# Kernel optimization log

Hardware: AMD Instinct MI355X
Metric: run time of the kernel (lower is better)

Reference implementation:

```python
import jax, jax.numpy as jnp
import numpy as np

N_NODES = 100000
N_EDGES = 1600000
N_GRAPHS = 256
K_HOPS = 3


def setup_inputs() -> dict:
    key = jax.random.key(0)
    ks = jax.random.split(key, 10)
    x = jax.random.normal(ks[0], (N_NODES, 32), dtype=jnp.float32)
    edge_index = jax.random.randint(ks[1], (2, N_EDGES), 0, N_NODES, dtype=jnp.int32)
    batch = jnp.sort(jax.random.randint(ks[2], (N_NODES,), 0, N_GRAPHS, dtype=jnp.int32))
    gcn_w = jax.random.normal(ks[3], (64, 32), dtype=jnp.float32) * 0.1
    gcn_b = jax.random.normal(ks[4], (64,), dtype=jnp.float32) * 0.1
    w1 = jax.random.normal(ks[5], (32, 64), dtype=jnp.float32) * 0.1
    b1 = jax.random.normal(ks[6], (32,), dtype=jnp.float32) * 0.1
    w2 = jax.random.normal(ks[7], (16, 32), dtype=jnp.float32) * 0.1
    b2 = jax.random.normal(ks[8], (16,), dtype=jnp.float32) * 0.1
    return {"x": x, "edge_index": edge_index, "batch": batch,
            "gcn_w": gcn_w, "gcn_b": gcn_b, "w1": w1, "b1": b1, "w2": w2, "b2": b2}


def reference(x, edge_index, batch, gcn_w, gcn_b, w1, b1, w2, b2):
    N = x.shape[0]
    src, dst = edge_index[0], edge_index[1]
    # GCN symmetric normalization with self-loops: deg = in-degree + 1
    deg = jax.ops.segment_sum(jnp.ones_like(src, dtype=x.dtype), dst, num_segments=N) + 1.0
    norm = deg ** -0.5  # [N]
    h = x
    for _ in range(K_HOPS):
        # edge message: norm[src] * h[src], scattered to dst, scaled by norm[dst];
        # self-loop contributes norm[i]^2 * h[i]
        msg = h[src] * norm[src][:, None]                     # [E, C]
        agg = jax.ops.segment_sum(msg, dst, num_segments=N)    # [N, C]
        h = norm[:, None] * agg + (norm * norm)[:, None] * h
    h = jax.nn.relu(h @ gcn_w.T + gcn_b)                       # [N, hidden]
    # global mean pool per graph
    counts = jax.ops.segment_sum(jnp.ones((N,), x.dtype), batch, num_segments=N_GRAPHS)
    sums = jax.ops.segment_sum(h, batch, num_segments=N_GRAPHS)
    h_avg = sums / jnp.maximum(counts, 1.0)[:, None]           # [G, hidden]
    # classifier (dropout = identity in eval)
    h1 = jax.nn.relu(h_avg @ w1.T + b1)
    logits = h1 @ w2.T + b2                                    # [G, nc]
    return logits
```

## Files before the change

### kernel.cpp

```cpp
#include <hip/hip_runtime.h>

constexpr int NW    = 391;
constexpr int CH    = 8192;
constexpr int CAP_B = 8192;
constexpr int CAP_C = 10240;

__device__ __forceinline__ unsigned bf16_rne(float x) {
    unsigned u = __float_as_uint(x);
    u += 0x7fffu + ((u >> 16) & 1u);
    return u >> 16;
}
__device__ __forceinline__ unsigned pack2(float even, float odd) {
    return bf16_rne(even) | (bf16_rne(odd) << 16);
}
__device__ __forceinline__ float lo_f(unsigned u) { return __uint_as_float(u << 16); }
__device__ __forceinline__ float hi_f(unsigned u) { return __uint_as_float(u & 0xffff0000u); }


__global__ __launch_bounds__(512) void k_bucket(const int* __restrict__ src,
                                                const int* __restrict__ dst, int E,
                                                int* __restrict__ wcur, int* __restrict__ packed) {
    __shared__ int h[256];
    __shared__ int base[256];
    int t = threadIdx.x;
    if (t < 256) h[t] = 0;
    __syncthreads();
    int b0 = blockIdx.x * CH;
    int cnt = min(CH, E - b0);
    for (int i = t; i < cnt; i += 512) atomicAdd(&h[dst[b0 + i] / NW], 1);
    __syncthreads();
    if (t < 256) { base[t] = atomicAdd(&wcur[t], h[t]); h[t] = 0; }
    __syncthreads();
    for (int i = t; i < cnt; i += 512) {
        int d = dst[b0 + i];
        int s = src[b0 + i];
        int w = d / NW;
        int l = d - w * NW;
        int r = atomicAdd(&h[w], 1);
        int pos = base[w] + r;
        if (pos < CAP_B) packed[w * CAP_B + pos] = (l << 17) | s;
    }
}


__global__ __launch_bounds__(512) void k_window(const int* __restrict__ packed,
                                                const int* __restrict__ wcur,
                                                float* __restrict__ norm,
                                                int2* __restrict__ rng,
                                                int* __restrict__ csr, int N, int W) {
    __shared__ int hist[NW];
    __shared__ int scan[512];
    __shared__ int cur[NW];
    int t = threadIdx.x, w = blockIdx.x;
    int lo = w * NW, nwn = min(NW, N - lo);
    for (int i = t; i < NW; i += 512) hist[i] = 0;
    __syncthreads();
    int cnt = min(wcur[w], CAP_B);
    const int* pk = packed + (size_t)w * CAP_B;
    for (int e = t; e < cnt; e += 512) atomicAdd(&hist[pk[e] >> 17], 1);
    __syncthreads();
    int d = (t < nwn) ? hist[t] : 0;
    if (t < nwn) norm[lo + t] = rsqrtf((float)(d + 1));
    int pd = (t < nwn) ? ((d + 7) & ~7) : 0;
    scan[t] = pd;
    __syncthreads();
    for (int s = 1; s < 512; s <<= 1) {
        int add = (t >= s) ? scan[t - s] : 0;
        __syncthreads();
        scan[t] += add;
        __syncthreads();
    }
    int base = w * CAP_C;
    int cend = base + scan[t];
    if (t < nwn) {
        rng[lo + t] = make_int2(cend - pd, cend);
        cur[t] = cend - pd;
    }
    if (w == W - 1 && t == 0) { norm[N] = 1.f; rng[N] = make_int2(0, 0); }
    __syncthreads();
    for (int e = t; e < cnt; e += 512) {
        int p = pk[e];
        int pos = atomicAdd(&cur[p >> 17], 1);
        csr[pos] = p & 0x1FFFF;
    }
    __syncthreads();
    if (t < nwn) {
        for (int pos = cur[t]; pos < cend; ++pos) csr[pos] = N;
    }
}


__global__ void k_prep(const float4* __restrict__ x, const float* __restrict__ norm,
                       uint2* __restrict__ outb, int N) {
    int t = blockIdx.x * blockDim.x + threadIdx.x;
    int i = t >> 3;
    if (i < N) {
        float n = norm[i];
        float4 v = x[t];
        outb[t] = make_uint2(pack2(v.x * n, v.y * n), pack2(v.z * n, v.w * n));
    } else if (i == N) {
        outb[t] = make_uint2(0u, 0u);
    }
}

template <bool LAST>
__global__ void k_hop(const uint2* __restrict__ tab, const float* __restrict__ norm,
                      const int2* __restrict__ rng, const int* __restrict__ csr,
                      uint2* __restrict__ outb, float4* __restrict__ outf, int N) {
    int group = (blockIdx.x * blockDim.x + threadIdx.x) >> 3;
    int l = threadIdx.x & 7;
    if (group > N) return;
    uint2 sv = tab[(size_t)group * 8 + l];
    float ax = lo_f(sv.x), ay = hi_f(sv.x), az = lo_f(sv.y), aw = hi_f(sv.y);
    int2 be = rng[group];
    for (int k = be.x; k < be.y; k += 8) {
        int e = csr[k + l];
        uint2 u[8];
#pragma unroll
        for (int j = 0; j < 8; ++j) {
            int s = __shfl(e, j, 8);
            u[j] = tab[(size_t)s * 8 + l];
        }
#pragma unroll
        for (int j = 0; j < 8; ++j) {
            ax += lo_f(u[j].x); ay += hi_f(u[j].x);
            az += lo_f(u[j].y); aw += hi_f(u[j].y);
        }
    }
    float n = norm[group];
    float sc = LAST ? n : n * n;
    ax *= sc; ay *= sc; az *= sc; aw *= sc;
    if (LAST) {
        if (group < N) outf[(size_t)group * 8 + l] = make_float4(ax, ay, az, aw);
    } else {
        outb[(size_t)group * 8 + l] = make_uint2(pack2(ax, ay), pack2(az, aw));
    }
}


__global__ __launch_bounds__(256) void k_feat(const float4* __restrict__ h4,
                                              const float* __restrict__ gw,
                                              const float* __restrict__ gb,
                                              float4* __restrict__ z4, int N) {
    __shared__ float w[64 * 32];
    __shared__ float bs[64];
    int t = threadIdx.x;
    for (int i = t; i < 64 * 32; i += 256) w[i] = gw[i];
    if (t < 64) bs[t] = gb[t];
    __syncthreads();
    int n = blockIdx.x * 256 + t;
    if (n >= N) return;
    float hrow[32];
    const float4* hr = h4 + (size_t)n * 8;
#pragma unroll
    for (int q = 0; q < 8; ++q) {
        float4 v = hr[q];
        hrow[q * 4] = v.x; hrow[q * 4 + 1] = v.y; hrow[q * 4 + 2] = v.z; hrow[q * 4 + 3] = v.w;
    }
#pragma unroll
    for (int c0 = 0; c0 < 64; c0 += 16) {
        float o[16];
#pragma unroll
        for (int cc = 0; cc < 16; ++cc) {
            const float* wr = &w[(c0 + cc) * 32];
            float d = bs[c0 + cc];
#pragma unroll
            for (int k = 0; k < 32; ++k) d += hrow[k] * wr[k];
            o[cc] = fmaxf(d, 0.f);
        }
#pragma unroll
        for (int q = 0; q < 4; ++q)
            z4[(size_t)n * 16 + (c0 >> 2) + q] =
                make_float4(o[q * 4], o[q * 4 + 1], o[q * 4 + 2], o[q * 4 + 3]);
    }
}


__global__ __launch_bounds__(256) void k_pool(const float4* __restrict__ z4,
                                              const int* __restrict__ batch, int N,
                                              const float* __restrict__ w1, const float* __restrict__ b1,
                                              const float* __restrict__ w2, const float* __restrict__ b2,
                                              float* __restrict__ out) {
    __shared__ float4 part[16][17];
    __shared__ float havg[64];
    __shared__ float h1s[32];
    __shared__ int se[2];
    int t = threadIdx.x, g = blockIdx.x;
    if (t < 2) {
        int target = g + t;
        int lo = 0, hi = N;
        while (lo < hi) { int mid = (lo + hi) >> 1; if (batch[mid] < target) lo = mid + 1; else hi = mid; }
        se[t] = lo;
    }
    __syncthreads();
    int start = se[0], end = se[1];
    int q = t & 15;
    int r = t >> 4;
    float4 acc = make_float4(0.f, 0.f, 0.f, 0.f);
    for (int n = start + r; n < end; n += 16) {
        float4 v = z4[(size_t)n * 16 + q];
        acc.x += v.x; acc.y += v.y; acc.z += v.z; acc.w += v.w;
    }
    part[r][q] = acc;
    __syncthreads();
#pragma unroll
    for (int s = 8; s > 0; s >>= 1) {
        if (r < s) {
            float4 a = part[r][q], b = part[r + s][q];
            a.x += b.x; a.y += b.y; a.z += b.z; a.w += b.w;
            part[r][q] = a;
        }
        __syncthreads();
    }
    if (t < 16) {
        int cnt = end - start;
        float inv = 1.f / (float)(cnt > 0 ? cnt : 1);
        float4 a = part[0][t];
        havg[t * 4] = a.x * inv; havg[t * 4 + 1] = a.y * inv;
        havg[t * 4 + 2] = a.z * inv; havg[t * 4 + 3] = a.w * inv;
    }
    __syncthreads();
    if (t < 32) {
        float d = b1[t];
#pragma unroll
        for (int k = 0; k < 64; ++k) d += havg[k] * w1[t * 64 + k];
        h1s[t] = fmaxf(d, 0.f);
    }
    __syncthreads();
    if (t < 16) {
        float d = b2[t];
#pragma unroll
        for (int j = 0; j < 32; ++j) d += h1s[j] * w2[t * 32 + j];
        out[g * 16 + t] = d;
    }
}


extern "C" void kernel_launch(void* const* d_in, const int* in_sizes, int n_in,
                              void* d_out, int out_size, void* d_ws, size_t ws_size,
                              hipStream_t stream) {
    const float* x     = (const float*)d_in[0];
    const int*   ei    = (const int*)d_in[1];
    const int*   batch = (const int*)d_in[2];
    const float* gw    = (const float*)d_in[3];
    const float* gb    = (const float*)d_in[4];
    const float* w1    = (const float*)d_in[5];
    const float* b1    = (const float*)d_in[6];
    const float* w2    = (const float*)d_in[7];
    const float* b2    = (const float*)d_in[8];
    float* out = (float*)d_out;

    int N = in_sizes[2];
    int E = in_sizes[1] / 2;
    int G = out_size / 16;
    const int* srcp = ei;
    const int* dstp = ei + E;

    int W  = (N + NW - 1) / NW;
    int NB = (E + CH - 1) / CH;

    char* ws = (char*)d_ws;
    size_t off = 0;
    auto alloc = [&](size_t bytes) -> void* {
        void* p = ws + off;
        off += (bytes + 255) & ~(size_t)255;
        return p;
    };
    int*   wcur   = (int*)alloc(256 * 4);
    int*   packed = (int*)alloc((size_t)W * CAP_B * 4);
    int*   csr    = (int*)alloc((size_t)W * CAP_C * 4);
    int2*  rng    = (int2*)alloc((size_t)(N + 1) * 8);
    float* norm   = (float*)alloc((size_t)(N + 1) * 4);
    uint2* hbA    = (uint2*)alloc((size_t)(N + 1) * 64);
    uint2* hbB    = (uint2*)alloc((size_t)(N + 1) * 64);
    float* hf     = (float*)alloc((size_t)N * 32 * 4);
    float* zbuf   = (float*)alloc((size_t)N * 64 * 4);

    hipMemsetAsync(wcur, 0, 256 * 4, stream);

    int pb = ((N + 1) * 8 + 255) / 256;

    k_bucket<<<NB, 512, 0, stream>>>(srcp, dstp, E, wcur, packed);
    k_window<<<W, 512, 0, stream>>>(packed, wcur, norm, rng, csr, N, W);

    k_prep<<<pb, 256, 0, stream>>>((const float4*)x, norm, hbA, N);
    k_hop<false><<<pb, 256, 0, stream>>>(hbA, norm, rng, csr, hbB, nullptr, N);
    k_hop<false><<<pb, 256, 0, stream>>>(hbB, norm, rng, csr, hbA, nullptr, N);
    k_hop<true ><<<pb, 256, 0, stream>>>(hbA, norm, rng, csr, nullptr, (float4*)hf, N);

    k_feat<<<(N + 255) / 256, 256, 0, stream>>>((const float4*)hf, gw, gb, (float4*)zbuf, N);
    k_pool<<<G, 256, 0, stream>>>((const float4*)zbuf, batch, N, w1, b1, w2, b2, out);
}
```

Before: 218.2 us.

## Vectorize bucketing loads, unroll hop gather by 16, store intermediates in bf16

The bucketing kernel now reads dst/src as int4 vectors for full chunks. The hop kernel gathers 16 neighbors per iteration to keep more loads in flight. The last hop, the feature transform output and the pooling input are all stored as bf16 instead of fp32, which halves the traffic of those intermediate buffers. This adds rounding error in the final hop and activations.

```diff
diff --git a/kernel.cpp b/kernel.cpp
--- a/kernel.cpp
+++ b/kernel.cpp
@@ -27,18 +27,46 @@
     __syncthreads();
     int b0 = blockIdx.x * CH;
     int cnt = min(CH, E - b0);
-    for (int i = t; i < cnt; i += 512) atomicAdd(&h[dst[b0 + i] / NW], 1);
+    if (cnt == CH) {
+        const int4* d4 = (const int4*)(dst + b0);
+        for (int i = t; i < CH / 4; i += 512) {
+            int4 v = d4[i];
+            atomicAdd(&h[v.x / NW], 1); atomicAdd(&h[v.y / NW], 1);
+            atomicAdd(&h[v.z / NW], 1); atomicAdd(&h[v.w / NW], 1);
+        }
+    } else {
+        for (int i = t; i < cnt; i += 512) atomicAdd(&h[dst[b0 + i] / NW], 1);
+    }
     __syncthreads();
     if (t < 256) { base[t] = atomicAdd(&wcur[t], h[t]); h[t] = 0; }
     __syncthreads();
-    for (int i = t; i < cnt; i += 512) {
-        int d = dst[b0 + i];
-        int s = src[b0 + i];
-        int w = d / NW;
-        int l = d - w * NW;
-        int r = atomicAdd(&h[w], 1);
-        int pos = base[w] + r;
-        if (pos < CAP_B) packed[w * CAP_B + pos] = (l << 17) | s;
+    if (cnt == CH) {
+        const int4* d4 = (const int4*)(dst + b0);
+        const int4* s4 = (const int4*)(src + b0);
+        for (int i = t; i < CH / 4; i += 512) {
+            int4 dv = d4[i];
+            int4 sv = s4[i];
+            int da[4] = {dv.x, dv.y, dv.z, dv.w};
+            int sa[4] = {sv.x, sv.y, sv.z, sv.w};
+#pragma unroll
+            for (int j = 0; j < 4; ++j) {
+                int w = da[j] / NW;
+                int l = da[j] - w * NW;
+                int r = atomicAdd(&h[w], 1);
+                int pos = base[w] + r;
+                if (pos < CAP_B) packed[w * CAP_B + pos] = (l << 17) | sa[j];
+            }
+        }
+    } else {
+        for (int i = t; i < cnt; i += 512) {
+            int d = dst[b0 + i];
+            int s = src[b0 + i];
+            int w = d / NW;
+            int l = d - w * NW;
+            int r = atomicAdd(&h[w], 1);
+            int pos = base[w] + r;
+            if (pos < CAP_B) packed[w * CAP_B + pos] = (l << 17) | s;
+        }
     }
 }
 
@@ -106,14 +134,35 @@
 template <bool LAST>
 __global__ void k_hop(const uint2* __restrict__ tab, const float* __restrict__ norm,
                       const int2* __restrict__ rng, const int* __restrict__ csr,
-                      uint2* __restrict__ outb, float4* __restrict__ outf, int N) {
+                      uint2* __restrict__ outb, int N) {
     int group = (blockIdx.x * blockDim.x + threadIdx.x) >> 3;
     int l = threadIdx.x & 7;
     if (group > N) return;
     uint2 sv = tab[(size_t)group * 8 + l];
     float ax = lo_f(sv.x), ay = hi_f(sv.x), az = lo_f(sv.y), aw = hi_f(sv.y);
     int2 be = rng[group];
-    for (int k = be.x; k < be.y; k += 8) {
+    int k = be.x;
+    for (; k + 16 <= be.y; k += 16) {
+        int e0 = csr[k + l];
+        int e1 = csr[k + 8 + l];
+        uint2 u[16];
+#pragma unroll
+        for (int j = 0; j < 8; ++j) {
+            int s = __shfl(e0, j, 8);
+            u[j] = tab[(size_t)s * 8 + l];
+        }
+#pragma unroll
+        for (int j = 0; j < 8; ++j) {
+            int s = __shfl(e1, j, 8);
+            u[8 + j] = tab[(size_t)s * 8 + l];
+        }
+#pragma unroll
+        for (int j = 0; j < 16; ++j) {
+            ax += lo_f(u[j].x); ay += hi_f(u[j].x);
+            az += lo_f(u[j].y); aw += hi_f(u[j].y);
+        }
+    }
+    if (k < be.y) {
         int e = csr[k + l];
         uint2 u[8];
 #pragma unroll
@@ -129,19 +178,14 @@
     }
     float n = norm[group];
     float sc = LAST ? n : n * n;
-    ax *= sc; ay *= sc; az *= sc; aw *= sc;
-    if (LAST) {
-        if (group < N) outf[(size_t)group * 8 + l] = make_float4(ax, ay, az, aw);
-    } else {
-        outb[(size_t)group * 8 + l] = make_uint2(pack2(ax, ay), pack2(az, aw));
-    }
-}
-
-
-__global__ __launch_bounds__(256) void k_feat(const float4* __restrict__ h4,
+    outb[(size_t)group * 8 + l] = make_uint2(pack2(ax * sc, ay * sc), pack2(az * sc, aw * sc));
+}
+
+
+__global__ __launch_bounds__(256) void k_feat(const uint2* __restrict__ hb,
                                               const float* __restrict__ gw,
                                               const float* __restrict__ gb,
-                                              float4* __restrict__ z4, int N) {
+                                              uint4* __restrict__ zb4, int N) {
     __shared__ float w[64 * 32];
     __shared__ float bs[64];
     int t = threadIdx.x;
@@ -151,11 +195,12 @@
     int n = blockIdx.x * 256 + t;
     if (n >= N) return;
     float hrow[32];
-    const float4* hr = h4 + (size_t)n * 8;
+    const uint2* hr = hb + (size_t)n * 8;
 #pragma unroll
     for (int q = 0; q < 8; ++q) {
-        float4 v = hr[q];
-        hrow[q * 4] = v.x; hrow[q * 4 + 1] = v.y; hrow[q * 4 + 2] = v.z; hrow[q * 4 + 3] = v.w;
+        uint2 u = hr[q];
+        hrow[q * 4] = lo_f(u.x); hrow[q * 4 + 1] = hi_f(u.x);
+        hrow[q * 4 + 2] = lo_f(u.y); hrow[q * 4 + 3] = hi_f(u.y);
     }
 #pragma unroll
     for (int c0 = 0; c0 < 64; c0 += 16) {
@@ -168,15 +213,15 @@
             for (int k = 0; k < 32; ++k) d += hrow[k] * wr[k];
             o[cc] = fmaxf(d, 0.f);
         }
-#pragma unroll
-        for (int q = 0; q < 4; ++q)
-            z4[(size_t)n * 16 + (c0 >> 2) + q] =
-                make_float4(o[q * 4], o[q * 4 + 1], o[q * 4 + 2], o[q * 4 + 3]);
-    }
-}
-
-
-__global__ __launch_bounds__(256) void k_pool(const float4* __restrict__ z4,
+        zb4[(size_t)n * 8 + (c0 >> 3)] =
+            make_uint4(pack2(o[0], o[1]), pack2(o[2], o[3]), pack2(o[4], o[5]), pack2(o[6], o[7]));
+        zb4[(size_t)n * 8 + (c0 >> 3) + 1] =
+            make_uint4(pack2(o[8], o[9]), pack2(o[10], o[11]), pack2(o[12], o[13]), pack2(o[14], o[15]));
+    }
+}
+
+
+__global__ __launch_bounds__(256) void k_pool(const uint2* __restrict__ zb2,
                                               const int* __restrict__ batch, int N,
                                               const float* __restrict__ w1, const float* __restrict__ b1,
                                               const float* __restrict__ w2, const float* __restrict__ b2,
@@ -198,8 +243,8 @@
     int r = t >> 4;
     float4 acc = make_float4(0.f, 0.f, 0.f, 0.f);
     for (int n = start + r; n < end; n += 16) {
-        float4 v = z4[(size_t)n * 16 + q];
-        acc.x += v.x; acc.y += v.y; acc.z += v.z; acc.w += v.w;
+        uint2 v = zb2[(size_t)n * 16 + q];
+        acc.x += lo_f(v.x); acc.y += hi_f(v.x); acc.z += lo_f(v.y); acc.w += hi_f(v.y);
     }
     part[r][q] = acc;
     __syncthreads();
@@ -273,8 +318,7 @@
     float* norm   = (float*)alloc((size_t)(N + 1) * 4);
     uint2* hbA    = (uint2*)alloc((size_t)(N + 1) * 64);
     uint2* hbB    = (uint2*)alloc((size_t)(N + 1) * 64);
-    float* hf     = (float*)alloc((size_t)N * 32 * 4);
-    float* zbuf   = (float*)alloc((size_t)N * 64 * 4);
+    unsigned* zbuf = (unsigned*)alloc((size_t)N * 64 * 2);
 
     hipMemsetAsync(wcur, 0, 256 * 4, stream);
 
@@ -284,10 +328,10 @@
     k_window<<<W, 512, 0, stream>>>(packed, wcur, norm, rng, csr, N, W);
 
     k_prep<<<pb, 256, 0, stream>>>((const float4*)x, norm, hbA, N);
-    k_hop<false><<<pb, 256, 0, stream>>>(hbA, norm, rng, csr, hbB, nullptr, N);
-    k_hop<false><<<pb, 256, 0, stream>>>(hbB, norm, rng, csr, hbA, nullptr, N);
-    k_hop<true ><<<pb, 256, 0, stream>>>(hbA, norm, rng, csr, nullptr, (float4*)hf, N);
-
-    k_feat<<<(N + 255) / 256, 256, 0, stream>>>((const float4*)hf, gw, gb, (float4*)zbuf, N);
-    k_pool<<<G, 256, 0, stream>>>((const float4*)zbuf, batch, N, w1, b1, w2, b2, out);
-}
+    k_hop<false><<<pb, 256, 0, stream>>>(hbA, norm, rng, csr, hbB, N);
+    k_hop<false><<<pb, 256, 0, stream>>>(hbB, norm, rng, csr, hbA, N);
+    k_hop<true ><<<pb, 256, 0, stream>>>(hbA, norm, rng, csr, hbB, N);
+
+    k_feat<<<(N + 255) / 256, 256, 0, stream>>>(hbB, gw, gb, (uint4*)zbuf, N);
+    k_pool<<<G, 256, 0, stream>>>((const uint2*)zbuf, batch, N, w1, b1, w2, b2, out);
+}
```

New measurement: 203.8 us. 1.07x faster.
